# Optimization experiments

Hardware: AMD Instinct MI355X
Metric: run time of the kernel (lower is better)

## Reference

```python
import jax, jax.numpy as jnp
import numpy as np

SENSORS = 50000
X_DIM = 64
HID = 64
Y_DIM = 32
N_EDGES = 800000


def setup_inputs() -> dict:
    key = jax.random.key(0)
    k0, k1, k2, k3 = jax.random.split(key, 4)
    x_input = jax.random.normal(k0, (1, X_DIM, SENSORS), dtype=jnp.float32)
    edge_index = jax.random.randint(k1, (2, N_EDGES), 0, SENSORS, dtype=jnp.int32)
    # GCNConv parameters (glorot-ish scaling)
    W1 = jax.random.normal(k2, (X_DIM, HID), dtype=jnp.float32) / np.sqrt(X_DIM)
    b1 = jnp.zeros((HID,), dtype=jnp.float32)
    W2 = jax.random.normal(k3, (HID, Y_DIM), dtype=jnp.float32) / np.sqrt(HID)
    b2 = jnp.zeros((Y_DIM,), dtype=jnp.float32)
    return {"x_input": x_input, "W1": W1, "b1": b1, "W2": W2, "b2": b2,
            "edge_index": edge_index}


def _gcn_conv(x, W, b, src, dst, n_nodes):
    """PyG GCNConv: x' = D^{-1/2}(A+I)D^{-1/2} (x W) + b."""
    h = x @ W  # [N, F_out]
    loop = jnp.arange(n_nodes, dtype=src.dtype)
    s = jnp.concatenate([src, loop])  # add self-loops
    d = jnp.concatenate([dst, loop])
    deg = jax.ops.segment_sum(jnp.ones_like(d, dtype=h.dtype), d,
                              num_segments=n_nodes)
    dinv = jnp.where(deg > 0, jax.lax.rsqrt(deg), 0.0)
    norm = dinv[s] * dinv[d]  # [E+N]
    msg = h[s] * norm[:, None]  # gather source features, scale
    out = jax.ops.segment_sum(msg, d, num_segments=n_nodes)  # scatter-add to targets
    return out + b


def reference(x_input, W1, b1, W2, b2, edge_index):
    B = x_input.shape[0]
    # [B, x, S] -> [B, S, x] -> [B*S, x]
    h = jnp.transpose(x_input, (0, 2, 1)).reshape(-1, X_DIM)
    n_nodes = h.shape[0]
    src, dst = edge_index[0], edge_index[1]
    h = _gcn_conv(h, W1, b1, src, dst, n_nodes)
    h = jax.nn.relu(h)
    h = _gcn_conv(h, W2, b2, src, dst, n_nodes)
    # [B*S, y] -> [B, S, y] -> [B, y, S]
    return jnp.transpose(h.reshape(B, SENSORS, Y_DIM), (0, 2, 1))
```

## Files before the change

kernel.cpp:

```cpp
#include <hip/hip_runtime.h>

#define NS 50000
#define NE 800000
#define XD 64
#define HD 64
#define YD 32

#define SHIFT 7
#define BNODES 128
#define NBUCK 391
#define BCAP 2560
#define NBLKA 256
#define EPB (NE / NBLKA)
#define SCAP 32

__device__ __forceinline__ unsigned f2b(float f) {
    union { float f; unsigned u; } c; c.f = f;
    return (c.u + 0x7fffu + ((c.u >> 16) & 1u)) >> 16;
}
__device__ __forceinline__ float blo(unsigned u) {
    union { unsigned u; float f; } c; c.u = u << 16; return c.f;
}
__device__ __forceinline__ float bhi(unsigned u) {
    union { unsigned u; float f; } c; c.u = u & 0xffff0000u; return c.f;
}

__global__ __launch_bounds__(256) void k_bucket(const int* __restrict__ src,
                                                const int* __restrict__ dst,
                                                int* __restrict__ cnt2,
                                                unsigned* __restrict__ ebuf2) {
    __shared__ unsigned se[EPB];
    __shared__ unsigned short lp[EPB];
    __shared__ int hist[NBUCK];
    int t = threadIdx.x, blk = blockIdx.x;
    int lo = blk * EPB;
    for (int i = t; i < NBUCK; i += 256) hist[i] = 0;
    __syncthreads();
    for (int i = t; i < EPB; i += 256) {
        unsigned d = (unsigned)__builtin_nontemporal_load(dst + lo + i);
        unsigned s = (unsigned)__builtin_nontemporal_load(src + lo + i);
        se[i] = (d << 16) | s;
        lp[i] = (unsigned short)atomicAdd(&hist[d >> SHIFT], 1);
    }
    __syncthreads();
    for (int i = t; i < NBUCK; i += 256)
        cnt2[blk * NBUCK + i] = min(hist[i], SCAP);
    for (int i = t; i < EPB; i += 256) {
        unsigned p = se[i];
        int b = p >> (16 + SHIFT);
        int pos = lp[i];
        if (pos < SCAP)
            ebuf2[((size_t)b * NBLKA + blk) * SCAP + pos] = p;
    }
}

__global__ __launch_bounds__(256) void k_sortxw1(const unsigned* __restrict__ ebuf2,
                                                 const int* __restrict__ cnt2,
                                                 unsigned short* __restrict__ csr,
                                                 int* __restrict__ beg,
                                                 int* __restrict__ endp,
                                                 float* __restrict__ dinv,
                                                 const float* __restrict__ x,
                                                 const float* __restrict__ W1,
                                                 unsigned* __restrict__ G1h) {
    __shared__ float w1[XD * HD];
    __shared__ unsigned se[BCAP];
    __shared__ unsigned short lcsr[BCAP];
    __shared__ int cnt[BNODES];
    __shared__ int offl[BNODES];
    __shared__ int cur[BNODES];
    __shared__ int sm[256];
    __shared__ int ntot;
    int b = blockIdx.x, t = threadIdx.x;
    for (int i = t; i < XD * HD; i += 256) w1[i] = W1[i];
    int c = cnt2[t * NBUCK + b];
    sm[t] = c;
    __syncthreads();
    int val = c;
    for (int o = 1; o < 256; o <<= 1) {
        int other = (t >= o) ? sm[t - o] : 0;
        __syncthreads();
        val += other;
        sm[t] = val;
        __syncthreads();
    }
    int soff = val - c;
    if (t == 255) ntot = val;
    if (t < BNODES) cnt[t] = 0;
    __syncthreads();
    int n = min(ntot, BCAP);
    {
        const unsigned* sb = ebuf2 + ((size_t)b * NBLKA + t) * SCAP;
        for (int j = 0; j < c; j += 4) {
            uint4 v = *(const uint4*)&sb[j];
            int p = soff + j;
            if (p < BCAP) se[p] = v.x;
            if (j + 1 < c && p + 1 < BCAP) se[p + 1] = v.y;
            if (j + 2 < c && p + 2 < BCAP) se[p + 2] = v.z;
            if (j + 3 < c && p + 3 < BCAP) se[p + 3] = v.w;
        }
    }
    __syncthreads();
    for (int i = t; i < n; i += 256) atomicAdd(&cnt[(se[i] >> 16) & (BNODES - 1)], 1);
    __syncthreads();
    int v = (t < BNODES) ? cnt[t] : 0;
    sm[t] = v;
    __syncthreads();
    int val2 = v;
    for (int o = 1; o < BNODES; o <<= 1) {
        int other = (t >= o) ? sm[t - o] : 0;
        __syncthreads();
        val2 += other;
        sm[t] = val2;
        __syncthreads();
    }
    if (t < BNODES) { offl[t] = val2 - v; cur[t] = val2 - v; }
    __syncthreads();
    for (int i = t; i < n; i += 256) {
        unsigned p = se[i];
        int l = (p >> 16) & (BNODES - 1);
        int pos = atomicAdd(&cur[l], 1);
        lcsr[pos] = (unsigned short)(p & 0xffffu);
    }
    __syncthreads();
    unsigned* gc = (unsigned*)(csr + (size_t)b * BCAP);
    int nw = (n + 1) >> 1;
    for (int i = t; i < nw; i += 256) gc[i] = ((const unsigned*)lcsr)[i];
    if (t < BNODES) {
        int node = b * BNODES + t;
        if (node < NS) {
            int bg = b * BCAP + offl[t];
            beg[node] = bg;
            endp[node] = bg + cnt[t];
            dinv[node] = rsqrtf((float)cnt[t] + 1.0f);
        }
    }
    int half = t >> 7, tn = t & (BNODES - 1);
    int node = b * BNODES + tn;
    if (node >= NS) return;
    float4 acc[8];
#pragma unroll
    for (int i = 0; i < 8; ++i) acc[i] = make_float4(0.f, 0.f, 0.f, 0.f);
    for (int xf = 0; xf < XD; ++xf) {
        float xv = __builtin_nontemporal_load(&x[(size_t)xf * NS + node]);
        const float4* wr = (const float4*)&w1[xf * HD + half * 32];
#pragma unroll
        for (int i = 0; i < 8; ++i) {
            float4 wv = wr[i];
            acc[i].x += xv * wv.x; acc[i].y += xv * wv.y;
            acc[i].z += xv * wv.z; acc[i].w += xv * wv.w;
        }
    }
    float dv = rsqrtf((float)cnt[tn] + 1.0f);
    unsigned pk[16];
#pragma unroll
    for (int i = 0; i < 8; ++i) {
        pk[2 * i]     = f2b(dv * acc[i].x) | (f2b(dv * acc[i].y) << 16);
        pk[2 * i + 1] = f2b(dv * acc[i].z) | (f2b(dv * acc[i].w) << 16);
    }
    uint4* o = (uint4*)&G1h[(size_t)node * 32 + half * 16];
#pragma unroll
    for (int i = 0; i < 4; ++i) o[i] = ((uint4*)pk)[i];
}

__global__ __launch_bounds__(256) void k_g1l2(const int* __restrict__ beg,
                                              const int* __restrict__ endp,
                                              const unsigned short* __restrict__ csr,
                                              const unsigned* __restrict__ G1h,
                                              const float* __restrict__ dinv,
                                              const float* __restrict__ b1,
                                              const float* __restrict__ W2,
                                              unsigned* __restrict__ G2h) {
    __shared__ float w2s[HD * YD];
    __shared__ float bsh[HD];
    __shared__ float lds_h[16][68];
    __shared__ float lds_dv[16];
    int t = threadIdx.x;
    for (int i = t; i < HD * YD; i += 256) w2s[i] = W2[i];
    if (t < HD) bsh[t] = b1[t];
    __syncthreads();

    int nl = t >> 4;
    int l  = t & 15;
    int node = blockIdx.x * 16 + nl;
    int beg_ = beg[node], end_ = endp[node];
    float a0 = 0.f, a1 = 0.f, a2 = 0.f, a3 = 0.f;
#pragma unroll 4
    for (int e = beg_; e < end_; ++e) {
        int s = (int)csr[e];
        uint2 u = *(const uint2*)&G1h[(unsigned)s * 32u + 2u * l];
        a0 += blo(u.x); a1 += bhi(u.x);
        a2 += blo(u.y); a3 += bhi(u.y);
    }
    uint2 us = *(const uint2*)&G1h[(unsigned)node * 32u + 2u * l];
    float dv = dinv[node];
    float4 h;
    h.x = fmaxf(fmaf(dv, a0 + blo(us.x), bsh[4 * l + 0]), 0.f);
    h.y = fmaxf(fmaf(dv, a1 + bhi(us.x), bsh[4 * l + 1]), 0.f);
    h.z = fmaxf(fmaf(dv, a2 + blo(us.y), bsh[4 * l + 2]), 0.f);
    h.w = fmaxf(fmaf(dv, a3 + bhi(us.y), bsh[4 * l + 3]), 0.f);
    *(float4*)&lds_h[nl][4 * l] = h;
    if (l == 0) lds_dv[nl] = dv;
    __syncthreads();

    int n2 = t >> 4;
    int oo = (t & 15) * 2;
    float dv2 = lds_dv[n2];
    const float* hr = &lds_h[n2][0];
    float p0 = 0.f, p1 = 0.f;
#pragma unroll
    for (int f4 = 0; f4 < 16; ++f4) {
        float4 hv = *(const float4*)&hr[f4 * 4];
        float2 wa = *(const float2*)&w2s[(f4 * 4 + 0) * YD + oo];
        float2 wb = *(const float2*)&w2s[(f4 * 4 + 1) * YD + oo];
        float2 wc = *(const float2*)&w2s[(f4 * 4 + 2) * YD + oo];
        float2 wd = *(const float2*)&w2s[(f4 * 4 + 3) * YD + oo];
        p0 = fmaf(hv.x, wa.x, p0); p1 = fmaf(hv.x, wa.y, p1);
        p0 = fmaf(hv.y, wb.x, p0); p1 = fmaf(hv.y, wb.y, p1);
        p0 = fmaf(hv.z, wc.x, p0); p1 = fmaf(hv.z, wc.y, p1);
        p0 = fmaf(hv.w, wd.x, p0); p1 = fmaf(hv.w, wd.y, p1);
    }
    int node2 = blockIdx.x * 16 + n2;
    G2h[(size_t)node2 * 16 + (t & 15)] = f2b(dv2 * p0) | (f2b(dv2 * p1) << 16);
}

__global__ __launch_bounds__(256) void k_g2out(const int* __restrict__ beg,
                                               const int* __restrict__ endp,
                                               const unsigned short* __restrict__ csr,
                                               const unsigned* __restrict__ G2h,
                                               const float* __restrict__ dinv,
                                               const float* __restrict__ b2,
                                               float* __restrict__ out) {
    __shared__ float ot[32][33];
    __shared__ float b2s[YD];
    int t = threadIdx.x;
    if (t < YD) b2s[t] = b2[t];
    int g = t >> 3;
    int l = t & 7;
    int base_n = blockIdx.x * 32;
    int node = base_n + g;
    if (node < NS) {
        int beg_ = beg[node], end_ = endp[node];
        float a0 = 0.f, a1 = 0.f, a2 = 0.f, a3 = 0.f;
#pragma unroll 4
        for (int e = beg_; e < end_; ++e) {
            int s = (int)csr[e];
            uint2 u = *(const uint2*)&G2h[(unsigned)s * 16u + 2u * l];
            a0 += blo(u.x); a1 += bhi(u.x);
            a2 += blo(u.y); a3 += bhi(u.y);
        }
        uint2 us = *(const uint2*)&G2h[(unsigned)node * 16u + 2u * l];
        float dv = dinv[node];
        ot[g][4 * l + 0] = dv * (a0 + blo(us.x));
        ot[g][4 * l + 1] = dv * (a1 + bhi(us.x));
        ot[g][4 * l + 2] = dv * (a2 + blo(us.y));
        ot[g][4 * l + 3] = dv * (a3 + bhi(us.y));
    }
    __syncthreads();
#pragma unroll
    for (int k = 0; k < 4; ++k) {
        int idx = k * 256 + t;
        int o = idx >> 5, n = idx & 31;
        int nd = base_n + n;
        if (nd < NS)
            out[(size_t)o * NS + nd] = ot[n][o] + b2s[o];
    }
}

extern "C" void kernel_launch(void* const* d_in, const int* in_sizes, int n_in,
                              void* d_out, int out_size, void* d_ws, size_t ws_size,
                              hipStream_t stream) {
    const float* x  = (const float*)d_in[0];
    const float* W1 = (const float*)d_in[1];
    const float* b1 = (const float*)d_in[2];
    const float* W2 = (const float*)d_in[3];
    const float* b2 = (const float*)d_in[4];
    const int* ei   = (const int*)d_in[5];
    const int* src = ei;
    const int* dst = ei + NE;

    int* cnt2      = (int*)d_ws;
    unsigned* ebuf2 = (unsigned*)(cnt2 + NBLKA * NBUCK);
    unsigned short* csr = (unsigned short*)(ebuf2 + (size_t)NBUCK * NBLKA * SCAP);
    int* beg      = (int*)((unsigned*)csr + (size_t)NBUCK * BCAP / 2);
    int* endp     = beg + 50000;
    float* dinv   = (float*)(endp + 50000);
    unsigned* G1h = (unsigned*)(dinv + 50000);
    unsigned* G2h = G1h + (size_t)50000 * 32;
    float* out    = (float*)d_out;

    k_bucket<<<NBLKA, 256, 0, stream>>>(src, dst, cnt2, ebuf2);
    k_sortxw1<<<NBUCK, 256, 0, stream>>>(ebuf2, cnt2, csr, beg, endp, dinv, x, W1, G1h);
    k_g1l2<<<NS / 16, 256, 0, stream>>>(beg, endp, csr, G1h, dinv, b1, W2, G2h);
    k_g2out<<<(NS + 31) / 32, 256, 0, stream>>>(beg, endp, csr, G2h, dinv, b2, out);
}
```

Before: 84.89 us.

## Move X·W1 GEMM into bucketing kernel and rescale by dinv in sort

```diff
diff --git a/kernel.cpp b/kernel.cpp
--- a/kernel.cpp
+++ b/kernel.cpp
@@ -13,6 +13,7 @@
 #define NBLKA 256
 #define EPB (NE / NBLKA)
 #define SCAP 32
+#define XW_BLKS ((NS + 255) / 256)
 
 __device__ __forceinline__ unsigned f2b(float f) {
     union { float f; unsigned u; } c; c.f = f;
@@ -25,88 +26,119 @@
     union { unsigned u; float f; } c; c.u = u & 0xffff0000u; return c.f;
 }
 
-__global__ __launch_bounds__(256) void k_bucket(const int* __restrict__ src,
+__global__ __launch_bounds__(256) void k_bktxw1(const int* __restrict__ src,
                                                 const int* __restrict__ dst,
                                                 int* __restrict__ cnt2,
-                                                unsigned* __restrict__ ebuf2) {
+                                                unsigned* __restrict__ ebuf2,
+                                                const float* __restrict__ x,
+                                                const float* __restrict__ W1,
+                                                unsigned* __restrict__ G1h) {
     __shared__ unsigned se[EPB];
     __shared__ unsigned short lp[EPB];
     __shared__ int hist[NBUCK];
-    int t = threadIdx.x, blk = blockIdx.x;
-    int lo = blk * EPB;
-    for (int i = t; i < NBUCK; i += 256) hist[i] = 0;
-    __syncthreads();
-    for (int i = t; i < EPB; i += 256) {
-        unsigned d = (unsigned)__builtin_nontemporal_load(dst + lo + i);
-        unsigned s = (unsigned)__builtin_nontemporal_load(src + lo + i);
-        se[i] = (d << 16) | s;
-        lp[i] = (unsigned short)atomicAdd(&hist[d >> SHIFT], 1);
-    }
-    __syncthreads();
-    for (int i = t; i < NBUCK; i += 256)
-        cnt2[blk * NBUCK + i] = min(hist[i], SCAP);
-    for (int i = t; i < EPB; i += 256) {
-        unsigned p = se[i];
-        int b = p >> (16 + SHIFT);
-        int pos = lp[i];
-        if (pos < SCAP)
-            ebuf2[((size_t)b * NBLKA + blk) * SCAP + pos] = p;
-    }
-}
-
-__global__ __launch_bounds__(256) void k_sortxw1(const unsigned* __restrict__ ebuf2,
-                                                 const int* __restrict__ cnt2,
-                                                 unsigned short* __restrict__ csr,
-                                                 int* __restrict__ beg,
-                                                 int* __restrict__ endp,
-                                                 float* __restrict__ dinv,
-                                                 const float* __restrict__ x,
-                                                 const float* __restrict__ W1,
-                                                 unsigned* __restrict__ G1h) {
-    __shared__ float w1[XD * HD];
+    __shared__ float w1f[XD * HD];
+    int t = threadIdx.x;
+    if (blockIdx.x < NBLKA) {
+        int blk = blockIdx.x;
+        int lo = blk * EPB;
+        for (int i = t; i < NBUCK; i += 256) hist[i] = 0;
+        __syncthreads();
+        for (int i = t; i < EPB; i += 256) {
+            unsigned d = (unsigned)__builtin_nontemporal_load(dst + lo + i);
+            unsigned s = (unsigned)__builtin_nontemporal_load(src + lo + i);
+            se[i] = (d << 16) | s;
+            lp[i] = (unsigned short)atomicAdd(&hist[d >> SHIFT], 1);
+        }
+        __syncthreads();
+        for (int i = t; i < NBUCK; i += 256)
+            cnt2[blk * NBUCK + i] = min(hist[i], SCAP);
+        for (int i = t; i < EPB; i += 256) {
+            unsigned p = se[i];
+            int b = p >> (16 + SHIFT);
+            int pos = lp[i];
+            if (pos < SCAP)
+                ebuf2[((size_t)b * NBLKA + blk) * SCAP + pos] = p;
+        }
+        return;
+    }
+    for (int i = t; i < XD * HD; i += 256) w1f[i] = W1[i];
+    __syncthreads();
+    int node = (blockIdx.x - NBLKA) * 256 + t;
+    if (node >= NS) return;
+    float4 acc[16];
+#pragma unroll
+    for (int i = 0; i < 16; ++i) acc[i] = make_float4(0.f, 0.f, 0.f, 0.f);
+    for (int xf = 0; xf < XD; ++xf) {
+        float xv = __builtin_nontemporal_load(&x[(size_t)xf * NS + node]);
+        const float4* wr = (const float4*)&w1f[xf * HD];
+#pragma unroll
+        for (int i = 0; i < 16; ++i) {
+            float4 wv = wr[i];
+            acc[i].x += xv * wv.x; acc[i].y += xv * wv.y;
+            acc[i].z += xv * wv.z; acc[i].w += xv * wv.w;
+        }
+    }
+    unsigned pk[32];
+#pragma unroll
+    for (int i = 0; i < 16; ++i) {
+        pk[2 * i]     = f2b(acc[i].x) | (f2b(acc[i].y) << 16);
+        pk[2 * i + 1] = f2b(acc[i].z) | (f2b(acc[i].w) << 16);
+    }
+    uint4* o = (uint4*)&G1h[(size_t)node * 32];
+#pragma unroll
+    for (int i = 0; i < 8; ++i) o[i] = ((uint4*)pk)[i];
+}
+
+__global__ __launch_bounds__(256) void k_sort(const unsigned* __restrict__ ebuf2,
+                                              const int* __restrict__ cnt2,
+                                              unsigned short* __restrict__ csr,
+                                              int* __restrict__ beg,
+                                              int* __restrict__ endp,
+                                              float* __restrict__ dinv,
+                                              unsigned* __restrict__ G1h) {
     __shared__ unsigned se[BCAP];
     __shared__ unsigned short lcsr[BCAP];
     __shared__ int cnt[BNODES];
     __shared__ int offl[BNODES];
     __shared__ int cur[BNODES];
     __shared__ int sm[256];
-    __shared__ int ntot;
+    __shared__ int wsum[4];
     int b = blockIdx.x, t = threadIdx.x;
-    for (int i = t; i < XD * HD; i += 256) w1[i] = W1[i];
+    int lane = t & 63, w = t >> 6;
     int c = cnt2[t * NBUCK + b];
-    sm[t] = c;
-    __syncthreads();
-    int val = c;
-    for (int o = 1; o < 256; o <<= 1) {
-        int other = (t >= o) ? sm[t - o] : 0;
-        __syncthreads();
-        val += other;
-        sm[t] = val;
-        __syncthreads();
-    }
-    int soff = val - c;
-    if (t == 255) ntot = val;
+    int v = c;
+#pragma unroll
+    for (int d = 1; d < 64; d <<= 1) {
+        int o = __shfl_up(v, d);
+        if (lane >= d) v += o;
+    }
+    if (lane == 63) wsum[w] = v;
     if (t < BNODES) cnt[t] = 0;
     __syncthreads();
+    int wpre = 0;
+#pragma unroll
+    for (int i = 0; i < 4; ++i) wpre += (i < w) ? wsum[i] : 0;
+    int soff = wpre + v - c;
+    int ntot = wsum[0] + wsum[1] + wsum[2] + wsum[3];
     int n = min(ntot, BCAP);
     {
         const unsigned* sb = ebuf2 + ((size_t)b * NBLKA + t) * SCAP;
         for (int j = 0; j < c; j += 4) {
-            uint4 v = *(const uint4*)&sb[j];
+            uint4 vv = *(const uint4*)&sb[j];
             int p = soff + j;
-            if (p < BCAP) se[p] = v.x;
-            if (j + 1 < c && p + 1 < BCAP) se[p + 1] = v.y;
-            if (j + 2 < c && p + 2 < BCAP) se[p + 2] = v.z;
-            if (j + 3 < c && p + 3 < BCAP) se[p + 3] = v.w;
+            if (p < BCAP) se[p] = vv.x;
+            if (j + 1 < c && p + 1 < BCAP) se[p + 1] = vv.y;
+            if (j + 2 < c && p + 2 < BCAP) se[p + 2] = vv.z;
+            if (j + 3 < c && p + 3 < BCAP) se[p + 3] = vv.w;
         }
     }
     __syncthreads();
     for (int i = t; i < n; i += 256) atomicAdd(&cnt[(se[i] >> 16) & (BNODES - 1)], 1);
     __syncthreads();
-    int v = (t < BNODES) ? cnt[t] : 0;
-    sm[t] = v;
-    __syncthreads();
-    int val2 = v;
+    int v2 = (t < BNODES) ? cnt[t] : 0;
+    sm[t] = v2;
+    __syncthreads();
+    int val2 = v2;
     for (int o = 1; o < BNODES; o <<= 1) {
         int other = (t >= o) ? sm[t - o] : 0;
         __syncthreads();
@@ -114,7 +146,7 @@
         sm[t] = val2;
         __syncthreads();
     }
-    if (t < BNODES) { offl[t] = val2 - v; cur[t] = val2 - v; }
+    if (t < BNODES) { offl[t] = val2 - v2; cur[t] = val2 - v2; }
     __syncthreads();
     for (int i = t; i < n; i += 256) {
         unsigned p = se[i];
@@ -135,32 +167,20 @@
             dinv[node] = rsqrtf((float)cnt[t] + 1.0f);
         }
     }
-    int half = t >> 7, tn = t & (BNODES - 1);
+    int tn = t >> 1, hf = t & 1;
     int node = b * BNODES + tn;
     if (node >= NS) return;
-    float4 acc[8];
-#pragma unroll
-    for (int i = 0; i < 8; ++i) acc[i] = make_float4(0.f, 0.f, 0.f, 0.f);
-    for (int xf = 0; xf < XD; ++xf) {
-        float xv = __builtin_nontemporal_load(&x[(size_t)xf * NS + node]);
-        const float4* wr = (const float4*)&w1[xf * HD + half * 32];
-#pragma unroll
-        for (int i = 0; i < 8; ++i) {
-            float4 wv = wr[i];
-            acc[i].x += xv * wv.x; acc[i].y += xv * wv.y;
-            acc[i].z += xv * wv.z; acc[i].w += xv * wv.w;
-        }
-    }
     float dv = rsqrtf((float)cnt[tn] + 1.0f);
-    unsigned pk[16];
-#pragma unroll
-    for (int i = 0; i < 8; ++i) {
-        pk[2 * i]     = f2b(dv * acc[i].x) | (f2b(dv * acc[i].y) << 16);
-        pk[2 * i + 1] = f2b(dv * acc[i].z) | (f2b(dv * acc[i].w) << 16);
-    }
-    uint4* o = (uint4*)&G1h[(size_t)node * 32 + half * 16];
-#pragma unroll
-    for (int i = 0; i < 4; ++i) o[i] = ((uint4*)pk)[i];
+    uint4* row = (uint4*)&G1h[(size_t)node * 32 + hf * 16];
+#pragma unroll
+    for (int i = 0; i < 4; ++i) {
+        uint4 u = row[i];
+        u.x = f2b(dv * blo(u.x)) | (f2b(dv * bhi(u.x)) << 16);
+        u.y = f2b(dv * blo(u.y)) | (f2b(dv * bhi(u.y)) << 16);
+        u.z = f2b(dv * blo(u.z)) | (f2b(dv * bhi(u.z)) << 16);
+        u.w = f2b(dv * blo(u.w)) | (f2b(dv * bhi(u.w)) << 16);
+        row[i] = u;
+    }
 }
 
 __global__ __launch_bounds__(256) void k_g1l2(const int* __restrict__ beg,
@@ -289,8 +309,8 @@
     unsigned* G2h = G1h + (size_t)50000 * 32;
     float* out    = (float*)d_out;
 
-    k_bucket<<<NBLKA, 256, 0, stream>>>(src, dst, cnt2, ebuf2);
-    k_sortxw1<<<NBUCK, 256, 0, stream>>>(ebuf2, cnt2, csr, beg, endp, dinv, x, W1, G1h);
+    k_bktxw1<<<NBLKA + XW_BLKS, 256, 0, stream>>>(src, dst, cnt2, ebuf2, x, W1, G1h);
+    k_sort<<<NBUCK, 256, 0, stream>>>(ebuf2, cnt2, csr, beg, endp, dinv, G1h);
     k_g1l2<<<NS / 16, 256, 0, stream>>>(beg, endp, csr, G1h, dinv, b1, W2, G2h);
     k_g2out<<<(NS + 31) / 32, 256, 0, stream>>>(beg, endp, csr, G2h, dinv, b2, out);
 }
```

New measurement: 90.79 us. 6.9% more time.
